# Optimization experiments

Measured on AMD Instinct MI355X. Metric: run time of the kernel, lower is better.

The kernel has to match this reference:

```python
import jax, jax.numpy as jnp
import numpy as np

N = 100000      # nodes
E = 1200000     # edges
B = 128         # graphs
H = 64          # hidden
IN_DIM = 64
GN_EPS = 1e-5


def _gin(x, edge_index, w1, b1, w2, b2):
    # GINConv (eps=0): mlp(x + sum_{j in N(i)} x_j)
    agg = jax.ops.segment_sum(x[edge_index[0]], edge_index[1], num_segments=N)
    h = x + agg
    return jax.nn.relu(h @ w1 + b1) @ w2 + b2


def _graph_norm(x, batch, w, b, ms):
    # PyG GraphNorm: out = w * (x - ms*mean) / sqrt(var + eps) + b, per-graph stats
    ones = jnp.ones((x.shape[0],), x.dtype)
    cnt = jnp.maximum(jax.ops.segment_sum(ones, batch, num_segments=B), 1.0)[:, None]
    mean = jax.ops.segment_sum(x, batch, num_segments=B) / cnt
    out = x - ms * mean[batch]
    var = jax.ops.segment_sum(out * out, batch, num_segments=B) / cnt
    return out * (jax.lax.rsqrt(var + GN_EPS)[batch] * w) + b


def setup_inputs() -> dict:
    key = jax.random.key(0)
    ks = jax.random.split(key, 32)
    inp = {
        'x': jax.random.normal(ks[0], (N, IN_DIM), jnp.float32),
        'edge_index': jax.random.randint(ks[1], (2, E), 0, N, dtype=jnp.int32),
        'batch': jnp.sort(jax.random.randint(ks[2], (N,), 0, B, dtype=jnp.int32)),
        'u': jax.random.normal(ks[3], (B, 3), jnp.float32),
    }
    k = 4
    for i in range(3):
        fin = IN_DIM if i == 0 else H
        inp[f'w{i+1}a'] = jax.random.normal(ks[k], (fin, H), jnp.float32) / np.sqrt(fin); k += 1
        inp[f'b{i+1}a'] = jnp.zeros((H,), jnp.float32)
        inp[f'w{i+1}b'] = jax.random.normal(ks[k], (H, H), jnp.float32) / np.sqrt(H); k += 1
        inp[f'b{i+1}b'] = jnp.zeros((H,), jnp.float32)
        inp[f'gn{i+1}_w'] = jnp.ones((H,), jnp.float32)
        inp[f'gn{i+1}_b'] = jnp.zeros((H,), jnp.float32)
        inp[f'gn{i+1}_ms'] = jnp.ones((H,), jnp.float32)
    inp['gate_w'] = jax.random.normal(ks[k], (H, 1), jnp.float32) / np.sqrt(H); k += 1
    inp['gate_b'] = jnp.zeros((1,), jnp.float32)
    inp['hw1'] = jax.random.normal(ks[k], (3 * H + 3, H), jnp.float32) / np.sqrt(3 * H + 3); k += 1
    inp['hb1'] = jnp.zeros((H,), jnp.float32)
    inp['hw2'] = jax.random.normal(ks[k], (H, 1), jnp.float32) / np.sqrt(H); k += 1
    inp['hb2'] = jnp.zeros((1,), jnp.float32)
    return inp


def reference(x, edge_index, batch, u,
              w1a, b1a, w1b, b1b, gn1_w, gn1_b, gn1_ms,
              w2a, b2a, w2b, b2b, gn2_w, gn2_b, gn2_ms,
              w3a, b3a, w3b, b3b, gn3_w, gn3_b, gn3_ms,
              gate_w, gate_b, hw1, hb1, hw2, hb2):
    h1 = jax.nn.relu(_graph_norm(_gin(x, edge_index, w1a, b1a, w1b, b1b), batch, gn1_w, gn1_b, gn1_ms))
    h2 = jax.nn.relu(_graph_norm(_gin(h1, edge_index, w2a, b2a, w2b, b2b), batch, gn2_w, gn2_b, gn2_ms))
    h3 = jax.nn.relu(_graph_norm(_gin(h2, edge_index, w3a, b3a, w3b, b3b), batch, gn3_w, gn3_b, gn3_ms))
    h = h1 + h2 + h3

    # AttentionalAggregation: per-graph softmax over gate logits
    gate = h @ gate_w + gate_b                                      # [N,1]
    m = jax.ops.segment_max(gate, batch, num_segments=B)            # [B,1]
    ex = jnp.exp(gate - m[batch])
    den = jax.ops.segment_sum(ex, batch, num_segments=B)
    att = jax.ops.segment_sum((ex / den[batch]) * h, batch, num_segments=B)

    ones = jnp.ones((h.shape[0],), h.dtype)
    cnt = jnp.maximum(jax.ops.segment_sum(ones, batch, num_segments=B), 1.0)[:, None]
    mean_pool = jax.ops.segment_sum(h, batch, num_segments=B) / cnt
    max_pool = jax.ops.segment_max(h, batch, num_segments=B)

    z = jnp.concatenate([att, mean_pool, max_pool, u], axis=1)       # [B, 3H+3]
    out = jax.nn.relu(z @ hw1 + hb1) @ hw2 + hb2                     # head_cls
    return out.reshape(-1)
```

## Files before the change

### kernel.cpp

```cpp
#include <hip/hip_runtime.h>
#include <math.h>

#define HDIM 64
#define GN_EPS 1e-5f
#define MAXNB 512
#define APITCH 72

typedef __attribute__((ext_vector_type(8))) short bf16x8;
typedef __attribute__((ext_vector_type(4))) float f32x4;

__device__ __forceinline__ int lower_bound_i(const int* a, int n, int key){
  int lo = 0, hi = n;
  while (lo < hi){ int mid = (lo + hi) >> 1; if (a[mid] < key) lo = mid + 1; else hi = mid; }
  return lo;
}

__device__ __forceinline__ unsigned fenc(float x){
  unsigned b = __float_as_uint(x);
  return (b & 0x80000000u) ? ~b : (b | 0x80000000u);
}
__device__ __forceinline__ float fdec(unsigned u){
  unsigned b = (u & 0x80000000u) ? (u ^ 0x80000000u) : ~u;
  return __uint_as_float(b);
}

__device__ __forceinline__ unsigned short f2bf(float f){
  unsigned u = __float_as_uint(f);
  u += 0x7fffu + ((u >> 16) & 1u);
  return (unsigned short)(u >> 16);
}
__device__ __forceinline__ float bf2f(unsigned short h){
  return __uint_as_float(((unsigned)h) << 16);
}

__device__ __forceinline__ void addbf(float* a, uint4 v){
  a[0] += __uint_as_float(v.x << 16);
  a[1] += __uint_as_float(v.x & 0xffff0000u);
  a[2] += __uint_as_float(v.y << 16);
  a[3] += __uint_as_float(v.y & 0xffff0000u);
  a[4] += __uint_as_float(v.z << 16);
  a[5] += __uint_as_float(v.z & 0xffff0000u);
  a[6] += __uint_as_float(v.w << 16);
  a[7] += __uint_as_float(v.w & 0xffff0000u);
}

__global__ void k_prep(const int* __restrict__ dst, int* __restrict__ bcount, int E, int NB,
                       const float* __restrict__ Wa0, const float* __restrict__ Wb0,
                       const float* __restrict__ Wa1, const float* __restrict__ Wb1,
                       const float* __restrict__ Wa2, const float* __restrict__ Wb2,
                       short* __restrict__ wbf,
                       const int* __restrict__ batch, int N, int* __restrict__ gs, int B){
  int tid = threadIdx.x;
  if (blockIdx.x < 256){
    __shared__ int lh[MAXNB];
    for (int b = tid; b < NB; b += 256) lh[b] = 0;
    __syncthreads();
    for (int i = blockIdx.x * 256 + tid; i < E; i += 256 * 256)
      atomicAdd(&lh[dst[i] >> 8], 1);
    __syncthreads();
    for (int b = tid; b < NB; b += 256){ int c = lh[b]; if (c) atomicAdd(&bcount[b], c); }
  } else if (blockIdx.x < 262){
    int wi = blockIdx.x - 256;
    const float* Wsrc[6] = {Wa0, Wb0, Wa1, Wb1, Wa2, Wb2};
    const float* W = Wsrc[wi];
    short* hi = wbf + wi * 8192;
    short* lo = hi + 4096;
    for (int i = tid; i < 4096; i += 256){
      int k = i >> 6, j = i & 63;
      float v = W[i];
      unsigned short h = f2bf(v);
      hi[j * 64 + k] = (short)h;
      lo[j * 64 + k] = (short)f2bf(v - bf2f(h));
    }
  } else {
    for (int g = tid; g <= B; g += 256) gs[g] = lower_bound_i(batch, N, g);
  }
}

__global__ void k_cvt(const float* __restrict__ x, unsigned short* __restrict__ xb, int n16){
  int i = blockIdx.x * blockDim.x + threadIdx.x;
  if (i >= n16) return;
  float4 v = ((const float4*)x)[i];
  ushort4 o;
  o.x = f2bf(v.x); o.y = f2bf(v.y); o.z = f2bf(v.z); o.w = f2bf(v.w);
  ((ushort4*)xb)[i] = o;
}

__global__ void k_bscan(const int* __restrict__ bcount, int* __restrict__ bbase,
                        int* __restrict__ bcursor, int NB){
  __shared__ int sd[MAXNB];
  int tid = threadIdx.x;
  int v = (tid < NB) ? bcount[tid] : 0;
  sd[tid] = v; __syncthreads();
  for (int o = 1; o < MAXNB; o <<= 1){
    int t = (tid >= o) ? sd[tid - o] : 0;
    __syncthreads();
    sd[tid] += t;
    __syncthreads();
  }
  int excl = sd[tid] - v;
  if (tid < NB){ bbase[tid] = excl; bcursor[tid] = excl; }
  if (tid == NB - 1) bbase[NB] = excl + v;
}

#define RCHUNK 8192
__global__ void k_breorder(const int* __restrict__ src, const int* __restrict__ dst,
                           int* __restrict__ bcursor, int2* __restrict__ ebuf, int E, int NB){
  __shared__ int lh[MAXNB];
  __shared__ int lbase[MAXNB];
  int tid = threadIdx.x;
  int c0 = blockIdx.x * RCHUNK;
  for (int b = tid; b < NB; b += 256) lh[b] = 0;
  __syncthreads();
  for (int j = 0; j < RCHUNK / 256; j++){
    int i = c0 + j * 256 + tid;
    if (i < E) atomicAdd(&lh[dst[i] >> 8], 1);
  }
  __syncthreads();
  for (int b = tid; b < NB; b += 256){
    int c = lh[b];
    lbase[b] = c ? atomicAdd(&bcursor[b], c) : 0;
    lh[b] = 0;
  }
  __syncthreads();
  for (int j = 0; j < RCHUNK / 256; j++){
    int i = c0 + j * 256 + tid;
    if (i < E){
      int d = dst[i]; int b = d >> 8;
      int r = atomicAdd(&lh[b], 1);
      ebuf[lbase[b] + r] = make_int2(src[i], d);
    }
  }
}

__global__ void k_bucket_csr(const int2* __restrict__ ebuf, const int* __restrict__ bbase,
                             int* __restrict__ deg, int* __restrict__ offs,
                             int* __restrict__ csr, int N){
  __shared__ int lh[256];
  __shared__ int lsc[256];
  int b = blockIdx.x;
  int lo = b << 8;
  int nn = min(256, N - lo);
  int tid = threadIdx.x;
  lh[tid] = 0; __syncthreads();
  int es = bbase[b], ee = bbase[b + 1];
  for (int i = es + tid; i < ee; i += 256) atomicAdd(&lh[ebuf[i].y - lo], 1);
  __syncthreads();
  int v = lh[tid];
  lsc[tid] = v; __syncthreads();
  for (int o = 1; o < 256; o <<= 1){
    int t = (tid >= o) ? lsc[tid - o] : 0;
    __syncthreads();
    lsc[tid] += t;
    __syncthreads();
  }
  int excl = lsc[tid] - v;
  if (tid < nn){ deg[lo + tid] = v; offs[lo + tid] = es + excl; }
  __syncthreads();
  lh[tid] = es + excl;
  __syncthreads();
  for (int i = es + tid; i < ee; i += 256){
    int2 e = ebuf[i];
    int pos = atomicAdd(&lh[e.y - lo], 1);
    csr[pos] = e.x;
  }
}

__global__ __launch_bounds__(256) void k_agg(
    const unsigned short* __restrict__ Pb, const int* __restrict__ csr,
    const int* __restrict__ offs, const int* __restrict__ deg,
    float* __restrict__ G, int n){
  int tid = threadIdx.x;
  int wave_id = blockIdx.x * 4 + (tid >> 6);
  int lane = tid & 63;
  int sub = lane >> 3, l8 = lane & 7;
  int node = wave_id * 8 + sub;
  bool ok = node < n;
  int st = 0, cnt = 0;
  if (ok){ st = offs[node]; cnt = deg[node]; }
  const uint4* Pv = (const uint4*)Pb;
  float a[8];
  #pragma unroll
  for (int k = 0; k < 8; k++) a[k] = 0.f;
  if (ok) addbf(a, Pv[(size_t)node * 8 + l8]);
  int sbase = sub << 3;
  for (int base = 0; base < cnt; base += 8){
    int rem = cnt - base;
    int s = (l8 < rem) ? csr[st + base + l8] : 0;
    int m = min(rem, 8);
    int j = 0;
    for (; j + 4 <= m; j += 4){
      int s0 = __shfl(s, sbase | j);
      int s1 = __shfl(s, sbase | (j + 1));
      int s2 = __shfl(s, sbase | (j + 2));
      int s3 = __shfl(s, sbase | (j + 3));
      uint4 v0 = Pv[(size_t)s0 * 8 + l8];
      uint4 v1 = Pv[(size_t)s1 * 8 + l8];
      uint4 v2 = Pv[(size_t)s2 * 8 + l8];
      uint4 v3 = Pv[(size_t)s3 * 8 + l8];
      addbf(a, v0); addbf(a, v1); addbf(a, v2); addbf(a, v3);
    }
    for (; j < m; ++j){
      int sj = __shfl(s, sbase | j);
      addbf(a, Pv[(size_t)sj * 8 + l8]);
    }
  }
  if (ok){
    float4* Gp = (float4*)(G + (size_t)node * HDIM + l8 * 8);
    Gp[0] = make_float4(a[0], a[1], a[2], a[3]);
    Gp[1] = make_float4(a[4], a[5], a[6], a[7]);
  }
}

__global__ __launch_bounds__(256, 3) void k_mlp(
    float* __restrict__ G, const int* __restrict__ batch,
    const short* __restrict__ Wall,
    const float* __restrict__ B1, const float* __restrict__ B2,
    float* __restrict__ stats, int N){
  __shared__ short Ws[16384];
  __shared__ short Ah[64 * APITCH];
  __shared__ short Al[64 * APITCH];
  __shared__ float ssum[64], ssq[64];
  int tid = threadIdx.x;

  #pragma unroll
  for (int i = 0; i < 8; i++)
    ((float4*)Ws)[i * 256 + tid] = ((const float4*)Wall)[i * 256 + tid];

  int wv = tid >> 6, lane = tid & 63;
  int quad = lane >> 4, l15 = lane & 15;
  int rbase = wv << 4;
  float bb1[4], bb2[4];
  #pragma unroll
  for (int t = 0; t < 4; t++){ bb1[t] = B1[t * 16 + l15]; bb2[t] = B2[t * 16 + l15]; }

  int tile0 = blockIdx.x << 1;
  float4 r[4], r2[4];
  {
    int tb = tile0 << 6;
    #pragma unroll
    for (int ri = 0; ri < 4; ri++){
      int idx = ri * 256 + tid;
      int node = tb + (idx >> 4), f4 = idx & 15;
      r[ri] = make_float4(0.f, 0.f, 0.f, 0.f);
      if (node < N) r[ri] = ((const float4*)G)[(size_t)node * 16 + f4];
    }
  }

  for (int tt = 0; tt < 2; tt++){
    int t0 = (tile0 + tt) << 6;
    if (t0 >= N) break;

    #pragma unroll
    for (int ri = 0; ri < 4; ri++){
      int idx = ri * 256 + tid;
      int node = idx >> 4, f4 = idx & 15;
      float vv[4] = {r[ri].x, r[ri].y, r[ri].z, r[ri].w};
      short h[4], l[4];
      #pragma unroll
      for (int j = 0; j < 4; j++){
        unsigned short hh = f2bf(vv[j]);
        h[j] = (short)hh;
        l[j] = (short)f2bf(vv[j] - bf2f(hh));
      }
      *(short4*)(Ah + node * APITCH + f4 * 4) = make_short4(h[0], h[1], h[2], h[3]);
      *(short4*)(Al + node * APITCH + f4 * 4) = make_short4(l[0], l[1], l[2], l[3]);
    }
    if (tid < 64){ ssum[tid] = 0.f; ssq[tid] = 0.f; }
    __syncthreads();

    if (tt == 0){
      int tb = (tile0 + 1) << 6;
      #pragma unroll
      for (int ri = 0; ri < 4; ri++){
        int idx = ri * 256 + tid;
        int node = tb + (idx >> 4), f4 = idx & 15;
        r2[ri] = make_float4(0.f, 0.f, 0.f, 0.f);
        if (node < N) r2[ri] = ((const float4*)G)[(size_t)node * 16 + f4];
      }
    }

    f32x4 acc[4];
    #pragma unroll
    for (int t = 0; t < 4; t++) acc[t] = (f32x4){0.f, 0.f, 0.f, 0.f};
    #pragma unroll
    for (int kb = 0; kb < 2; kb++){
      int kk = kb * 32 + quad * 8;
      bf16x8 a_h = *(const bf16x8*)(Ah + (rbase + l15) * APITCH + kk);
      bf16x8 a_l = *(const bf16x8*)(Al + (rbase + l15) * APITCH + kk);
      #pragma unroll
      for (int t = 0; t < 4; t++){
        bf16x8 b_h = *(const bf16x8*)(Ws + (t * 16 + l15) * 64 + kk);
        bf16x8 b_l = *(const bf16x8*)(Ws + 4096 + (t * 16 + l15) * 64 + kk);
        acc[t] = __builtin_amdgcn_mfma_f32_16x16x32_bf16(a_h, b_h, acc[t], 0, 0, 0);
        acc[t] = __builtin_amdgcn_mfma_f32_16x16x32_bf16(a_h, b_l, acc[t], 0, 0, 0);
        acc[t] = __builtin_amdgcn_mfma_f32_16x16x32_bf16(a_l, b_h, acc[t], 0, 0, 0);
      }
    }
    __syncthreads();

    #pragma unroll
    for (int t = 0; t < 4; t++){
      #pragma unroll
      for (int rg = 0; rg < 4; rg++){
        float v = fmaxf(acc[t][rg] + bb1[t], 0.f);
        int row = rbase + quad * 4 + rg;
        int col = t * 16 + l15;
        unsigned short hh = f2bf(v);
        Ah[row * APITCH + col] = (short)hh;
        Al[row * APITCH + col] = (short)f2bf(v - bf2f(hh));
      }
    }
    __syncthreads();

    f32x4 acc2[4];
    #pragma unroll
    for (int t = 0; t < 4; t++) acc2[t] = (f32x4){0.f, 0.f, 0.f, 0.f};
    #pragma unroll
    for (int kb = 0; kb < 2; kb++){
      int kk = kb * 32 + quad * 8;
      bf16x8 a_h = *(const bf16x8*)(Ah + (rbase + l15) * APITCH + kk);
      bf16x8 a_l = *(const bf16x8*)(Al + (rbase + l15) * APITCH + kk);
      #pragma unroll
      for (int t = 0; t < 4; t++){
        bf16x8 b_h = *(const bf16x8*)(Ws + 8192 + (t * 16 + l15) * 64 + kk);
        bf16x8 b_l = *(const bf16x8*)(Ws + 12288 + (t * 16 + l15) * 64 + kk);
        acc2[t] = __builtin_amdgcn_mfma_f32_16x16x32_bf16(a_h, b_h, acc2[t], 0, 0, 0);
        acc2[t] = __builtin_amdgcn_mfma_f32_16x16x32_bf16(a_h, b_l, acc2[t], 0, 0, 0);
        acc2[t] = __builtin_amdgcn_mfma_f32_16x16x32_bf16(a_l, b_h, acc2[t], 0, 0, 0);
      }
    }

    int lastn = min(t0 + 63, N - 1);
    int g0 = batch[t0];
    bool uniform = (batch[lastn] == g0) && (t0 + 63 < N);
    #pragma unroll
    for (int t = 0; t < 4; t++){
      int f = t * 16 + l15;
      float s = 0.f, q = 0.f;
      #pragma unroll
      for (int rg = 0; rg < 4; rg++){
        float v = acc2[t][rg] + bb2[t];
        int node = t0 + rbase + quad * 4 + rg;
        if (node < N) G[(size_t)node * HDIM + f] = v;
        if (uniform){
          s += v; q += v * v;
        } else if (node < N){
          int g = batch[node];
          atomicAdd(&stats[g * 128 + f], v);
          atomicAdd(&stats[g * 128 + 64 + f], v * v);
        }
      }
      if (uniform){
        s += __shfl_xor(s, 16); s += __shfl_xor(s, 32);
        q += __shfl_xor(q, 16); q += __shfl_xor(q, 32);
        if (quad == 0){ atomicAdd(&ssum[f], s); atomicAdd(&ssq[f], q); }
      }
    }
    __syncthreads();
    if (uniform && tid < 64){
      atomicAdd(&stats[g0 * 128 + tid], ssum[tid]);
      atomicAdd(&stats[g0 * 128 + 64 + tid], ssq[tid]);
    }
    #pragma unroll
    for (int ri = 0; ri < 4; ri++) r[ri] = r2[ri];
  }
}

__global__ void k_gn_apply(const float* __restrict__ Y, const int* __restrict__ batch,
                           const float* __restrict__ stats, const int* __restrict__ gs,
                           const float* __restrict__ w, const float* __restrict__ ms,
                           const float* __restrict__ bias,
                           unsigned short* __restrict__ Cb, float* __restrict__ hsum, int n16,
                           int first, int writeC){
  int i = blockIdx.x * blockDim.x + threadIdx.x;
  if (i >= n16) return;
  int node = i >> 4, q = i & 15;
  int g = batch[node];
  float cnt = (float)max(gs[g + 1] - gs[g], 1);
  float4 y  = ((const float4*)Y)[i];
  float4 s1 = ((const float4*)(stats + g * 128))[q];
  float4 s2 = ((const float4*)(stats + g * 128 + 64))[q];
  float4 wv = ((const float4*)w)[q];
  float4 mv = ((const float4*)ms)[q];
  float4 bv = ((const float4*)bias)[q];
  float4 v;
  #define APPLY1(c) { \
    float mean = s1.c / cnt; float ex2 = s2.c / cnt; \
    float var = ex2 - (2.f * mv.c - mv.c * mv.c) * mean * mean; \
    float sc = rsqrtf(var + GN_EPS) * wv.c; \
    v.c = fmaxf((y.c - mv.c * mean) * sc + bv.c, 0.f); }
  APPLY1(x) APPLY1(y) APPLY1(z) APPLY1(w)
  #undef APPLY1
  if (writeC){
    ushort4 o;
    o.x = f2bf(v.x); o.y = f2bf(v.y); o.z = f2bf(v.z); o.w = f2bf(v.w);
    ((ushort4*)Cb)[i] = o;
  }
  if (first){
    ((float4*)hsum)[i] = v;
  } else {
    float4 h = ((float4*)hsum)[i];
    h.x += v.x; h.y += v.y; h.z += v.z; h.w += v.w;
    ((float4*)hsum)[i] = h;
  }
}

#define GN_NPW 32
__global__ void k_pool1(const float* __restrict__ HS, const int* __restrict__ batch,
                        const float* __restrict__ GW, const float* __restrict__ GB,
                        float* __restrict__ sumbuf, unsigned* __restrict__ maxbuf,
                        float* __restrict__ gatebuf, unsigned* __restrict__ gmaxbuf, int n){
  int wave = (int)((blockIdx.x * blockDim.x + threadIdx.x) >> 6);
  int lane = threadIdx.x & 63;
  int s = wave * GN_NPW;
  if (s >= n) return;
  int e = min(s + GN_NPW, n);
  float gwv = GW[lane];
  float gb = GB[0];
  int cur = batch[s];
  float macc = 0.f, xacc = -INFINITY, gmx = -INFINITY;
  for (int nd = s; nd < e; ++nd){
    int g = batch[nd];
    if (g != cur){
      atomicAdd(&sumbuf[cur * 64 + lane], macc);
      atomicMax(&maxbuf[cur * 64 + lane], fenc(xacc));
      if (lane == 0) atomicMax(&gmaxbuf[cur], fenc(gmx));
      macc = 0.f; xacc = -INFINITY; gmx = -INFINITY; cur = g;
    }
    float hv = HS[(size_t)nd * HDIM + lane];
    macc += hv; xacc = fmaxf(xacc, hv);
    float gv = hv * gwv;
    #pragma unroll
    for (int msk = 1; msk < 64; msk <<= 1) gv += __shfl_xor(gv, msk);
    gv += gb;
    if (lane == 0) gatebuf[nd] = gv;
    gmx = fmaxf(gmx, gv);
  }
  atomicAdd(&sumbuf[cur * 64 + lane], macc);
  atomicMax(&maxbuf[cur * 64 + lane], fenc(xacc));
  if (lane == 0) atomicMax(&gmaxbuf[cur], fenc(gmx));
}

__global__ void k_pool2(const float* __restrict__ HS, const int* __restrict__ batch,
                        const float* __restrict__ gatebuf, const unsigned* __restrict__ gmaxbuf,
                        float* __restrict__ attbuf, float* __restrict__ denbuf, int n){
  int wave = (int)((blockIdx.x * blockDim.x + threadIdx.x) >> 6);
  int lane = threadIdx.x & 63;
  int s = wave * GN_NPW;
  if (s >= n) return;
  int e = min(s + GN_NPW, n);
  int cur = batch[s];
  float m = fdec(gmaxbuf[cur]);
  float aacc = 0.f, dacc = 0.f;
  for (int nd = s; nd < e; ++nd){
    int g = batch[nd];
    if (g != cur){
      atomicAdd(&attbuf[cur * 64 + lane], aacc);
      if (lane == 0) atomicAdd(&denbuf[cur], dacc);
      aacc = 0.f; dacc = 0.f; cur = g; m = fdec(gmaxbuf[cur]);
    }
    float ex = expf(gatebuf[nd] - m);
    float hv = HS[(size_t)nd * HDIM + lane];
    aacc += ex * hv; dacc += ex;
  }
  atomicAdd(&attbuf[cur * 64 + lane], aacc);
  if (lane == 0) atomicAdd(&denbuf[cur], dacc);
}

__global__ void k_pool3(const float* __restrict__ attbuf, const float* __restrict__ denbuf,
                        const float* __restrict__ sumbuf, const unsigned* __restrict__ maxbuf,
                        const int* __restrict__ gs, const float* __restrict__ U,
                        const float* __restrict__ HW1, const float* __restrict__ HB1,
                        const float* __restrict__ HW2, const float* __restrict__ HB2,
                        float* __restrict__ out){
  __shared__ float z[200];
  int g = blockIdx.x;
  int tid = threadIdx.x;
  float cnt = (float)max(gs[g + 1] - gs[g], 1);
  float den = denbuf[g];
  z[tid]       = attbuf[g * 64 + tid] / den;
  z[64 + tid]  = sumbuf[g * 64 + tid] / cnt;
  z[128 + tid] = fdec(maxbuf[g * 64 + tid]);
  if (tid < 3) z[192 + tid] = U[g * 3 + tid];
  __syncthreads();
  float acc = HB1[tid];
  for (int k = 0; k < 195; k++) acc += z[k] * HW1[k * 64 + tid];
  float sv = fmaxf(acc, 0.f) * HW2[tid];
  #pragma unroll
  for (int msk = 1; msk < 64; msk <<= 1) sv += __shfl_xor(sv, msk);
  if (tid == 0) out[g] = sv + HB2[0];
}

extern "C" void kernel_launch(void* const* d_in, const int* in_sizes, int n_in,
                              void* d_out, int out_size, void* d_ws, size_t ws_size,
                              hipStream_t stream){
  const float* x     = (const float*)d_in[0];
  const int*   ei    = (const int*)d_in[1];
  const int*   batch = (const int*)d_in[2];
  const float* u     = (const float*)d_in[3];
  const float* W[3][4]; const float* GNp[3][3];
  for (int l = 0; l < 3; l++){
    int base = 4 + l * 7;
    W[l][0]  = (const float*)d_in[base + 0];
    W[l][1]  = (const float*)d_in[base + 1];
    W[l][2]  = (const float*)d_in[base + 2];
    W[l][3]  = (const float*)d_in[base + 3];
    GNp[l][0]= (const float*)d_in[base + 4];
    GNp[l][1]= (const float*)d_in[base + 5];
    GNp[l][2]= (const float*)d_in[base + 6];
  }
  const float* gate_w = (const float*)d_in[25];
  const float* gate_b = (const float*)d_in[26];
  const float* hw1    = (const float*)d_in[27];
  const float* hb1    = (const float*)d_in[28];
  const float* hw2    = (const float*)d_in[29];
  const float* hb2    = (const float*)d_in[30];
  float* out = (float*)d_out;

  int N = in_sizes[0] / HDIM;
  int E = in_sizes[1] / 2;
  int B = in_sizes[3] / 3;
  const int* src = ei;
  const int* dst = ei + E;
  int NB = (N + 255) >> 8;

  char* w8 = (char*)d_ws;
  size_t NH = (size_t)N * HDIM * sizeof(float);
  size_t NHb = (size_t)N * HDIM * sizeof(short);
  auto alignup = [](size_t v){ return (v + 255) & ~(size_t)255; };
  size_t off = 0;
  float* hsum    = (float*)(w8 + off); off += alignup(NH);
  float* G       = (float*)(w8 + off); off += alignup(NH);
  unsigned short* xb   = (unsigned short*)(w8 + off); off += alignup(NHb);
  unsigned short* bufA = (unsigned short*)(w8 + off); off += alignup(NHb);
  unsigned short* bufB = (unsigned short*)(w8 + off); off += alignup(NHb);
  float* gatebuf = (float*)(w8 + off); off += alignup((size_t)N * 4);
  int*   deg     = (int*)(w8 + off);   off += alignup((size_t)N * 4);
  int*   offs    = (int*)(w8 + off);   off += alignup((size_t)N * 4);
  int*   csr     = (int*)(w8 + off);   off += alignup((size_t)E * 4);
  int2*  ebuf    = (int2*)(w8 + off);  off += alignup((size_t)E * 8);
  int*   bcount  = (int*)(w8 + off);   off += alignup((size_t)(MAXNB + 1) * 4);
  int*   bbase   = (int*)(w8 + off);   off += alignup((size_t)(MAXNB + 1) * 4);
  int*   bcursor = (int*)(w8 + off);   off += alignup((size_t)(MAXNB + 1) * 4);
  float* stats   = (float*)(w8 + off); off += alignup((size_t)3 * B * 128 * 4);
  float* poolz   = (float*)(w8 + off);
  size_t poolz_bytes = ((size_t)B * 64 * 3 + 2 * B) * 4;
  off += alignup(poolz_bytes);
  float*    sumbuf  = poolz;
  unsigned* maxbuf  = (unsigned*)(poolz + (size_t)B * 64);
  float*    attbuf  = poolz + (size_t)2 * B * 64;
  float*    denbuf  = poolz + (size_t)3 * B * 64;
  unsigned* gmaxbuf = (unsigned*)(poolz + (size_t)3 * B * 64 + B);
  int*   gs      = (int*)(w8 + off);   off += alignup((size_t)(B + 1) * 4);
  short* wbf     = (short*)(w8 + off); off += alignup((size_t)6 * 8192 * 2);
  (void)ws_size; (void)n_in; (void)out_size;

  hipMemsetAsync(stats, 0, (size_t)3 * B * 128 * 4, stream);
  hipMemsetAsync(poolz, 0, poolz_bytes, stream);
  hipMemsetAsync(bcount, 0, (size_t)(MAXNB + 1) * 4, stream);

  const int tb = 256;
  int n16 = N * 16;
  k_prep<<<263, tb, 0, stream>>>(dst, bcount, E, NB,
                                 W[0][0], W[0][2], W[1][0], W[1][2], W[2][0], W[2][2],
                                 wbf, batch, N, gs, B);
  k_cvt<<<(n16 + tb - 1) / tb, tb, 0, stream>>>(x, xb, n16);
  k_bscan<<<1, MAXNB, 0, stream>>>(bcount, bbase, bcursor, NB);
  k_breorder<<<(E + RCHUNK - 1) / RCHUNK, tb, 0, stream>>>(src, dst, bcursor, ebuf, E, NB);
  k_bucket_csr<<<NB, tb, 0, stream>>>(ebuf, bbase, deg, offs, csr, N);

  int nwaves = (N + GN_NPW - 1) / GN_NPW;
  int segblocks = (nwaves * 64 + tb - 1) / tb;
  int nblk64 = (N + 63) >> 6;
  int nblk2 = (nblk64 + 1) >> 1;
  int aggwaves = (N + 7) >> 3;
  int aggblocks = (aggwaves + 3) >> 2;

  const unsigned short* P = xb;
  unsigned short* C = bufA;
  for (int l = 0; l < 3; l++){
    k_agg<<<aggblocks, 256, 0, stream>>>(P, csr, offs, deg, G, N);
    float* lstats = stats + (size_t)l * B * 128;
    k_mlp<<<nblk2, 256, 0, stream>>>(G, batch, wbf + (size_t)l * 16384,
                                     W[l][1], W[l][3], lstats, N);
    k_gn_apply<<<(n16 + tb - 1) / tb, tb, 0, stream>>>(G, batch, lstats, gs,
                                                       GNp[l][0], GNp[l][2], GNp[l][1],
                                                       C, hsum, n16, l == 0 ? 1 : 0,
                                                       l == 2 ? 0 : 1);
    P = C;
    C = (l == 0) ? bufB : bufA;
  }
  k_pool1<<<segblocks, tb, 0, stream>>>(hsum, batch, gate_w, gate_b,
                                        sumbuf, maxbuf, gatebuf, gmaxbuf, N);
  k_pool2<<<segblocks, tb, 0, stream>>>(hsum, batch, gatebuf, gmaxbuf, attbuf, denbuf, N);
  k_pool3<<<B, 64, 0, stream>>>(attbuf, denbuf, sumbuf, maxbuf, gs, u,
                                hw1, hb1, hw2, hb2, out);
}
```

Baseline: 496.1 us.

## Fuse preprocessing and trunk into two persistent cooperative kernels with grid sync

Measured after the change: 486.8 us. About the same (-1.9%).

```diff
diff --git a/kernel.cpp b/kernel.cpp
--- a/kernel.cpp
+++ b/kernel.cpp
@@ -1,10 +1,14 @@
 #include <hip/hip_runtime.h>
+#include <hip/hip_cooperative_groups.h>
 #include <math.h>
+
+namespace cg = cooperative_groups;
 
 #define HDIM 64
 #define GN_EPS 1e-5f
 #define MAXNB 512
 #define APITCH 72
+#define RCHUNK 8192
 
 typedef __attribute__((ext_vector_type(8))) short bf16x8;
 typedef __attribute__((ext_vector_type(4))) float f32x4;
@@ -14,7 +18,6 @@
   while (lo < hi){ int mid = (lo + hi) >> 1; if (a[mid] < key) lo = mid + 1; else hi = mid; }
   return lo;
 }
-
 __device__ __forceinline__ unsigned fenc(float x){
   unsigned b = __float_as_uint(x);
   return (b & 0x80000000u) ? ~b : (b | 0x80000000u);
@@ -23,7 +26,6 @@
   unsigned b = (u & 0x80000000u) ? (u ^ 0x80000000u) : ~u;
   return __uint_as_float(b);
 }
-
 __device__ __forceinline__ unsigned short f2bf(float f){
   unsigned u = __float_as_uint(f);
   u += 0x7fffu + ((u >> 16) & 1u);
@@ -32,7 +34,6 @@
 __device__ __forceinline__ float bf2f(unsigned short h){
   return __uint_as_float(((unsigned)h) << 16);
 }
-
 __device__ __forceinline__ void addbf(float* a, uint4 v){
   a[0] += __uint_as_float(v.x << 16);
   a[1] += __uint_as_float(v.x & 0xffff0000u);
@@ -42,6 +43,500 @@
   a[5] += __uint_as_float(v.z & 0xffff0000u);
   a[6] += __uint_as_float(v.w << 16);
   a[7] += __uint_as_float(v.w & 0xffff0000u);
+}
+
+struct BuildArgs {
+  const int* src; const int* dst; int E; int NB;
+  const float* W0; const float* W1; const float* W2;
+  const float* W3; const float* W4; const float* W5;
+  short* wbf;
+  const int* batch; int N; int* gs; int B;
+  int* bcount; int* bbase; int* bcursor;
+  int2* ebuf; int* deg; int* offs; int* csr;
+  const float* x; unsigned short* xb; int n16;
+  float* stats; int statsN; float* poolz; int poolzN;
+};
+
+__global__ void k_build(BuildArgs a){
+  cg::grid_group grid = cg::this_grid();
+  __shared__ int sA[512];
+  __shared__ int sB[512];
+  int tid = threadIdx.x;
+  int gsz = (int)gridDim.x;
+  int gstart = blockIdx.x * 256 + tid;
+  int gstride = gsz * 256;
+
+  for (int i = gstart; i <= MAXNB; i += gstride) a.bcount[i] = 0;
+  for (int i = gstart; i < a.statsN; i += gstride) a.stats[i] = 0.f;
+  for (int i = gstart; i < a.poolzN; i += gstride) a.poolz[i] = 0.f;
+  if (blockIdx.x < 6){
+    const float* Wsrc = (blockIdx.x == 0) ? a.W0 : (blockIdx.x == 1) ? a.W1 :
+                        (blockIdx.x == 2) ? a.W2 : (blockIdx.x == 3) ? a.W3 :
+                        (blockIdx.x == 4) ? a.W4 : a.W5;
+    short* hi = a.wbf + blockIdx.x * 8192;
+    short* lo = hi + 4096;
+    for (int i = tid; i < 4096; i += 256){
+      int k = i >> 6, j = i & 63;
+      float v = Wsrc[i];
+      unsigned short h = f2bf(v);
+      hi[j * 64 + k] = (short)h;
+      lo[j * 64 + k] = (short)f2bf(v - bf2f(h));
+    }
+  } else if (blockIdx.x == 6){
+    for (int g = tid; g <= a.B; g += 256) a.gs[g] = lower_bound_i(a.batch, a.N, g);
+  }
+  for (int i = gstart; i < a.n16; i += gstride){
+    float4 v = ((const float4*)a.x)[i];
+    ushort4 o;
+    o.x = f2bf(v.x); o.y = f2bf(v.y); o.z = f2bf(v.z); o.w = f2bf(v.w);
+    ((ushort4*)a.xb)[i] = o;
+  }
+  grid.sync();
+
+  for (int b = tid; b < a.NB; b += 256) sA[b] = 0;
+  __syncthreads();
+  for (int i = gstart; i < a.E; i += gstride) atomicAdd(&sA[a.dst[i] >> 8], 1);
+  __syncthreads();
+  for (int b = tid; b < a.NB; b += 256){ int c = sA[b]; if (c) atomicAdd(&a.bcount[b], c); }
+  grid.sync();
+
+  if (blockIdx.x == 0){
+    int v0 = (2 * tid     < a.NB) ? a.bcount[2 * tid]     : 0;
+    int v1 = (2 * tid + 1 < a.NB) ? a.bcount[2 * tid + 1] : 0;
+    int L = v0 + v1;
+    sB[tid] = L; __syncthreads();
+    for (int o = 1; o < 256; o <<= 1){
+      int tv = (tid >= o) ? sB[tid - o] : 0;
+      __syncthreads();
+      sB[tid] += tv;
+      __syncthreads();
+    }
+    int run = sB[tid] - L;
+    if (2 * tid < a.NB){ a.bbase[2 * tid] = run; a.bcursor[2 * tid] = run; }
+    run += v0;
+    if (2 * tid + 1 < a.NB){ a.bbase[2 * tid + 1] = run; a.bcursor[2 * tid + 1] = run; }
+    if (tid == 255) a.bbase[a.NB] = sB[255];
+  }
+  grid.sync();
+
+  int nch = (a.E + RCHUNK - 1) / RCHUNK;
+  for (int ci = blockIdx.x; ci < nch; ci += gsz){
+    int c0 = ci * RCHUNK;
+    for (int b = tid; b < a.NB; b += 256) sA[b] = 0;
+    __syncthreads();
+    for (int j = 0; j < RCHUNK / 256; j++){
+      int i = c0 + j * 256 + tid;
+      if (i < a.E) atomicAdd(&sA[a.dst[i] >> 8], 1);
+    }
+    __syncthreads();
+    for (int b = tid; b < a.NB; b += 256){
+      int c = sA[b];
+      sB[b] = c ? atomicAdd(&a.bcursor[b], c) : 0;
+      sA[b] = 0;
+    }
+    __syncthreads();
+    for (int j = 0; j < RCHUNK / 256; j++){
+      int i = c0 + j * 256 + tid;
+      if (i < a.E){
+        int d = a.dst[i]; int b = d >> 8;
+        int rr = atomicAdd(&sA[b], 1);
+        a.ebuf[sB[b] + rr] = make_int2(a.src[i], d);
+      }
+    }
+    __syncthreads();
+  }
+  grid.sync();
+
+  for (int b = blockIdx.x; b < a.NB; b += gsz){
+    int lo = b << 8;
+    int nn = min(256, a.N - lo);
+    sA[tid] = 0; __syncthreads();
+    int es = a.bbase[b], ee = a.bbase[b + 1];
+    for (int i = es + tid; i < ee; i += 256) atomicAdd(&sA[a.ebuf[i].y - lo], 1);
+    __syncthreads();
+    int v = sA[tid];
+    sB[tid] = v; __syncthreads();
+    for (int o = 1; o < 256; o <<= 1){
+      int tv = (tid >= o) ? sB[tid - o] : 0;
+      __syncthreads();
+      sB[tid] += tv;
+      __syncthreads();
+    }
+    int excl = sB[tid] - v;
+    if (tid < nn){ a.deg[lo + tid] = v; a.offs[lo + tid] = es + excl; }
+    __syncthreads();
+    sA[tid] = es + excl;
+    __syncthreads();
+    for (int i = es + tid; i < ee; i += 256){
+      int2 e = a.ebuf[i];
+      int pos = atomicAdd(&sA[e.y - lo], 1);
+      a.csr[pos] = e.x;
+    }
+    __syncthreads();
+  }
+}
+
+struct TrunkArgs {
+  const unsigned short* xb;
+  unsigned short* bufA; unsigned short* bufB;
+  float* G; float* hsum;
+  const int* csr; const int* offs; const int* deg; const int* batch; const int* gs;
+  const short* wbf;
+  const float* B1a; const float* B1b; const float* B1c;
+  const float* B2a; const float* B2b; const float* B2c;
+  const float* gnw0; const float* gnw1; const float* gnw2;
+  const float* gnb0; const float* gnb1; const float* gnb2;
+  const float* gnm0; const float* gnm1; const float* gnm2;
+  float* stats; int N; int n16; int B;
+  const float* gw; const float* gb; const float* u;
+  const float* hw1; const float* hb1; const float* hw2; const float* hb2;
+  float* sumbuf; unsigned* maxbuf; float* attbuf; float* denbuf; unsigned* gmaxbuf;
+  float* gatebuf; float* out;
+};
+
+__global__ __launch_bounds__(256, 3) void k_trunk(TrunkArgs a){
+  cg::grid_group grid = cg::this_grid();
+  __shared__ __align__(16) char smem[51712];
+  short* Ws  = (short*)smem;
+  short* Ah  = (short*)(smem + 32768);
+  short* Al  = (short*)(smem + 32768 + 9216);
+  float* ssum = (float*)(smem + 32768 + 18432);
+  float* ssq  = ssum + 64;
+  int tid = threadIdx.x;
+  int wv = tid >> 6, lane = tid & 63;
+  int gsz = (int)gridDim.x;
+  int N = a.N;
+  int ntile = (N + 63) >> 6;
+
+  const unsigned short* P = a.xb;
+  unsigned short* Cb = a.bufA;
+
+  for (int l = 0; l < 3; l++){
+    {
+      int sub = lane >> 3, l8 = lane & 7, sbase = sub << 3;
+      const uint4* Pv = (const uint4*)P;
+      int wid = blockIdx.x * 4 + wv;
+      int wstep = gsz * 4 * 8;
+      for (int nb = wid * 8; nb < N; nb += wstep){
+        int node = nb + sub;
+        bool ok = node < N;
+        int st = 0, cnt = 0;
+        if (ok){ st = a.offs[node]; cnt = a.deg[node]; }
+        float acc8[8];
+        #pragma unroll
+        for (int k = 0; k < 8; k++) acc8[k] = 0.f;
+        if (ok) addbf(acc8, Pv[(size_t)node * 8 + l8]);
+        for (int base = 0; base < cnt; base += 8){
+          int rem = cnt - base;
+          int s = (l8 < rem) ? a.csr[st + base + l8] : 0;
+          int m = min(rem, 8);
+          int j = 0;
+          for (; j + 4 <= m; j += 4){
+            int s0 = __shfl(s, sbase | j);
+            int s1 = __shfl(s, sbase | (j + 1));
+            int s2 = __shfl(s, sbase | (j + 2));
+            int s3 = __shfl(s, sbase | (j + 3));
+            uint4 v0 = Pv[(size_t)s0 * 8 + l8];
+            uint4 v1 = Pv[(size_t)s1 * 8 + l8];
+            uint4 v2 = Pv[(size_t)s2 * 8 + l8];
+            uint4 v3 = Pv[(size_t)s3 * 8 + l8];
+            addbf(acc8, v0); addbf(acc8, v1); addbf(acc8, v2); addbf(acc8, v3);
+          }
+          for (; j < m; ++j){
+            int sj = __shfl(s, sbase | j);
+            addbf(acc8, Pv[(size_t)sj * 8 + l8]);
+          }
+        }
+        if (ok){
+          float4* Gp = (float4*)(a.G + (size_t)node * HDIM + l8 * 8);
+          Gp[0] = make_float4(acc8[0], acc8[1], acc8[2], acc8[3]);
+          Gp[1] = make_float4(acc8[4], acc8[5], acc8[6], acc8[7]);
+        }
+      }
+    }
+    grid.sync();
+
+    {
+      const short* Wall = a.wbf + (size_t)l * 16384;
+      for (int j = tid; j < 2048; j += 256){
+        int p = j >> 9, rem = j & 511, rr = rem >> 3, c8 = rem & 7;
+        bf16x8 v = ((const bf16x8*)Wall)[j];
+        *(bf16x8*)(Ws + p * 4096 + rr * 64 + ((c8 ^ (rr & 7)) << 3)) = v;
+      }
+      int quad = lane >> 4, l15 = lane & 15;
+      int rbase = wv << 4;
+      int h7 = l15 & 7;
+      const float* B1 = (l == 0) ? a.B1a : (l == 1) ? a.B1b : a.B1c;
+      const float* B2 = (l == 0) ? a.B2a : (l == 1) ? a.B2b : a.B2c;
+      float bb1[4], bb2[4];
+      #pragma unroll
+      for (int t4 = 0; t4 < 4; t4++){ bb1[t4] = B1[t4 * 16 + l15]; bb2[t4] = B2[t4 * 16 + l15]; }
+      float* lstats = a.stats + (size_t)l * a.B * 128;
+
+      int t = blockIdx.x;
+      float4 r[4], r2[4];
+      #pragma unroll
+      for (int ri = 0; ri < 4; ri++){ r[ri] = make_float4(0.f,0.f,0.f,0.f); r2[ri] = r[ri]; }
+      if (t < ntile){
+        int tb = t << 6;
+        #pragma unroll
+        for (int ri = 0; ri < 4; ri++){
+          int idx = ri * 256 + tid;
+          int node = tb + (idx >> 4), f4 = idx & 15;
+          if (node < N) r[ri] = ((const float4*)a.G)[(size_t)node * 16 + f4];
+        }
+      }
+      while (t < ntile){
+        int t0 = t << 6;
+        #pragma unroll
+        for (int ri = 0; ri < 4; ri++){
+          int idx = ri * 256 + tid;
+          int nodeL = idx >> 4, f4 = idx & 15;
+          float vv[4] = {r[ri].x, r[ri].y, r[ri].z, r[ri].w};
+          short hh[4], ll[4];
+          #pragma unroll
+          for (int j = 0; j < 4; j++){
+            unsigned short hv = f2bf(vv[j]);
+            hh[j] = (short)hv;
+            ll[j] = (short)f2bf(vv[j] - bf2f(hv));
+          }
+          *(short4*)(Ah + nodeL * APITCH + f4 * 4) = make_short4(hh[0], hh[1], hh[2], hh[3]);
+          *(short4*)(Al + nodeL * APITCH + f4 * 4) = make_short4(ll[0], ll[1], ll[2], ll[3]);
+        }
+        if (tid < 64){ ssum[tid] = 0.f; ssq[tid] = 0.f; }
+        __syncthreads();
+
+        int tn = t + gsz;
+        #pragma unroll
+        for (int ri = 0; ri < 4; ri++) r2[ri] = make_float4(0.f,0.f,0.f,0.f);
+        if (tn < ntile){
+          int tb = tn << 6;
+          #pragma unroll
+          for (int ri = 0; ri < 4; ri++){
+            int idx = ri * 256 + tid;
+            int node = tb + (idx >> 4), f4 = idx & 15;
+            if (node < N) r2[ri] = ((const float4*)a.G)[(size_t)node * 16 + f4];
+          }
+        }
+
+        f32x4 acc[4];
+        #pragma unroll
+        for (int t4 = 0; t4 < 4; t4++) acc[t4] = (f32x4){0.f, 0.f, 0.f, 0.f};
+        #pragma unroll
+        for (int kb = 0; kb < 2; kb++){
+          int kk = kb * 32 + quad * 8;
+          int swz = ((kb * 4 + quad) ^ h7) << 3;
+          bf16x8 a_h = *(const bf16x8*)(Ah + (rbase + l15) * APITCH + kk);
+          bf16x8 a_l = *(const bf16x8*)(Al + (rbase + l15) * APITCH + kk);
+          #pragma unroll
+          for (int t4 = 0; t4 < 4; t4++){
+            int row = t4 * 16 + l15;
+            bf16x8 b_h = *(const bf16x8*)(Ws + row * 64 + swz);
+            bf16x8 b_l = *(const bf16x8*)(Ws + 4096 + row * 64 + swz);
+            acc[t4] = __builtin_amdgcn_mfma_f32_16x16x32_bf16(a_h, b_h, acc[t4], 0, 0, 0);
+            acc[t4] = __builtin_amdgcn_mfma_f32_16x16x32_bf16(a_h, b_l, acc[t4], 0, 0, 0);
+            acc[t4] = __builtin_amdgcn_mfma_f32_16x16x32_bf16(a_l, b_h, acc[t4], 0, 0, 0);
+          }
+        }
+        __syncthreads();
+
+        #pragma unroll
+        for (int t4 = 0; t4 < 4; t4++){
+          #pragma unroll
+          for (int rg = 0; rg < 4; rg++){
+            float v = fmaxf(acc[t4][rg] + bb1[t4], 0.f);
+            int row = rbase + quad * 4 + rg;
+            int col = t4 * 16 + l15;
+            unsigned short hv = f2bf(v);
+            Ah[row * APITCH + col] = (short)hv;
+            Al[row * APITCH + col] = (short)f2bf(v - bf2f(hv));
+          }
+        }
+        __syncthreads();
+
+        f32x4 acc2[4];
+        #pragma unroll
+        for (int t4 = 0; t4 < 4; t4++) acc2[t4] = (f32x4){0.f, 0.f, 0.f, 0.f};
+        #pragma unroll
+        for (int kb = 0; kb < 2; kb++){
+          int kk = kb * 32 + quad * 8;
+          int swz = ((kb * 4 + quad) ^ h7) << 3;
+          bf16x8 a_h = *(const bf16x8*)(Ah + (rbase + l15) * APITCH + kk);
+          bf16x8 a_l = *(const bf16x8*)(Al + (rbase + l15) * APITCH + kk);
+          #pragma unroll
+          for (int t4 = 0; t4 < 4; t4++){
+            int row = t4 * 16 + l15;
+            bf16x8 b_h = *(const bf16x8*)(Ws + 8192 + row * 64 + swz);
+            bf16x8 b_l = *(const bf16x8*)(Ws + 12288 + row * 64 + swz);
+            acc2[t4] = __builtin_amdgcn_mfma_f32_16x16x32_bf16(a_h, b_h, acc2[t4], 0, 0, 0);
+            acc2[t4] = __builtin_amdgcn_mfma_f32_16x16x32_bf16(a_h, b_l, acc2[t4], 0, 0, 0);
+            acc2[t4] = __builtin_amdgcn_mfma_f32_16x16x32_bf16(a_l, b_h, acc2[t4], 0, 0, 0);
+          }
+        }
+
+        int lastn = min(t0 + 63, N - 1);
+        int g0 = a.batch[t0];
+        bool uniform = (a.batch[lastn] == g0) && (t0 + 63 < N);
+        #pragma unroll
+        for (int t4 = 0; t4 < 4; t4++){
+          int f = t4 * 16 + l15;
+          float s = 0.f, q = 0.f;
+          #pragma unroll
+          for (int rg = 0; rg < 4; rg++){
+            float v = acc2[t4][rg] + bb2[t4];
+            int node = t0 + rbase + quad * 4 + rg;
+            if (node < N) a.G[(size_t)node * HDIM + f] = v;
+            if (uniform){
+              s += v; q += v * v;
+            } else if (node < N){
+              int g = a.batch[node];
+              atomicAdd(&lstats[g * 128 + f], v);
+              atomicAdd(&lstats[g * 128 + 64 + f], v * v);
+            }
+          }
+          if (uniform){
+            s += __shfl_xor(s, 16); s += __shfl_xor(s, 32);
+            q += __shfl_xor(q, 16); q += __shfl_xor(q, 32);
+            if (quad == 0){ atomicAdd(&ssum[f], s); atomicAdd(&ssq[f], q); }
+          }
+        }
+        __syncthreads();
+        if (uniform && tid < 64){
+          atomicAdd(&lstats[g0 * 128 + tid], ssum[tid]);
+          atomicAdd(&lstats[g0 * 128 + 64 + tid], ssq[tid]);
+        }
+        #pragma unroll
+        for (int ri = 0; ri < 4; ri++) r[ri] = r2[ri];
+        t = tn;
+      }
+    }
+    grid.sync();
+
+    {
+      const float* wv_ = (l == 0) ? a.gnw0 : (l == 1) ? a.gnw1 : a.gnw2;
+      const float* bv_ = (l == 0) ? a.gnb0 : (l == 1) ? a.gnb1 : a.gnb2;
+      const float* mv_ = (l == 0) ? a.gnm0 : (l == 1) ? a.gnm1 : a.gnm2;
+      const float* lstats = a.stats + (size_t)l * a.B * 128;
+      int first = (l == 0) ? 1 : 0;
+      int writeC = (l == 2) ? 0 : 1;
+      for (int i = blockIdx.x * 256 + tid; i < a.n16; i += gsz * 256){
+        int node = i >> 4, q = i & 15;
+        int g = a.batch[node];
+        float cnt = (float)max(a.gs[g + 1] - a.gs[g], 1);
+        float4 y  = ((const float4*)a.G)[i];
+        float4 s1 = ((const float4*)(lstats + g * 128))[q];
+        float4 s2 = ((const float4*)(lstats + g * 128 + 64))[q];
+        float4 wq = ((const float4*)wv_)[q];
+        float4 mq = ((const float4*)mv_)[q];
+        float4 bq = ((const float4*)bv_)[q];
+        float4 v;
+        #define APPLY1(c) { \
+          float mean = s1.c / cnt; float ex2 = s2.c / cnt; \
+          float var = ex2 - (2.f * mq.c - mq.c * mq.c) * mean * mean; \
+          float sc = rsqrtf(var + GN_EPS) * wq.c; \
+          v.c = fmaxf((y.c - mq.c * mean) * sc + bq.c, 0.f); }
+        APPLY1(x) APPLY1(y) APPLY1(z) APPLY1(w)
+        #undef APPLY1
+        if (writeC){
+          ushort4 o;
+          o.x = f2bf(v.x); o.y = f2bf(v.y); o.z = f2bf(v.z); o.w = f2bf(v.w);
+          ((ushort4*)Cb)[i] = o;
+        }
+        if (first){
+          ((float4*)a.hsum)[i] = v;
+        } else {
+          float4 h = ((float4*)a.hsum)[i];
+          h.x += v.x; h.y += v.y; h.z += v.z; h.w += v.w;
+          ((float4*)a.hsum)[i] = h;
+        }
+      }
+    }
+    grid.sync();
+    P = Cb;
+    Cb = (l == 0) ? a.bufB : a.bufA;
+  }
+
+  {
+    int nchunk = (N + 31) >> 5;
+    int wid = blockIdx.x * 4 + wv;
+    float gwv = a.gw[lane];
+    float gb = a.gb[0];
+    for (int c = wid; c < nchunk; c += gsz * 4){
+      int s = c << 5, e = min(s + 32, N);
+      int cur = a.batch[s];
+      float macc = 0.f, xacc = -INFINITY, gmx = -INFINITY;
+      for (int nd = s; nd < e; ++nd){
+        int g = a.batch[nd];
+        if (g != cur){
+          atomicAdd(&a.sumbuf[cur * 64 + lane], macc);
+          atomicMax(&a.maxbuf[cur * 64 + lane], fenc(xacc));
+          if (lane == 0) atomicMax(&a.gmaxbuf[cur], fenc(gmx));
+          macc = 0.f; xacc = -INFINITY; gmx = -INFINITY; cur = g;
+        }
+        float hv = a.hsum[(size_t)nd * HDIM + lane];
+        macc += hv; xacc = fmaxf(xacc, hv);
+        float gv = hv * gwv;
+        #pragma unroll
+        for (int msk = 1; msk < 64; msk <<= 1) gv += __shfl_xor(gv, msk);
+        gv += gb;
+        if (lane == 0) a.gatebuf[nd] = gv;
+        gmx = fmaxf(gmx, gv);
+      }
+      atomicAdd(&a.sumbuf[cur * 64 + lane], macc);
+      atomicMax(&a.maxbuf[cur * 64 + lane], fenc(xacc));
+      if (lane == 0) atomicMax(&a.gmaxbuf[cur], fenc(gmx));
+    }
+  }
+  grid.sync();
+
+  {
+    int nchunk = (N + 31) >> 5;
+    int wid = blockIdx.x * 4 + wv;
+    for (int c = wid; c < nchunk; c += gsz * 4){
+      int s = c << 5, e = min(s + 32, N);
+      int cur = a.batch[s];
+      float m = fdec(a.gmaxbuf[cur]);
+      float aacc = 0.f, dacc = 0.f;
+      for (int nd = s; nd < e; ++nd){
+        int g = a.batch[nd];
+        if (g != cur){
+          atomicAdd(&a.attbuf[cur * 64 + lane], aacc);
+          if (lane == 0) atomicAdd(&a.denbuf[cur], dacc);
+          aacc = 0.f; dacc = 0.f; cur = g; m = fdec(a.gmaxbuf[cur]);
+        }
+        float ex = expf(a.gatebuf[nd] - m);
+        float hv = a.hsum[(size_t)nd * HDIM + lane];
+        aacc += ex * hv; dacc += ex;
+      }
+      atomicAdd(&a.attbuf[cur * 64 + lane], aacc);
+      if (lane == 0) atomicAdd(&a.denbuf[cur], dacc);
+    }
+  }
+  grid.sync();
+
+  {
+    float* z = (float*)smem;
+    int g = blockIdx.x;
+    if (g < a.B){
+      float cnt = (float)max(a.gs[g + 1] - a.gs[g], 1);
+      if (tid < 64){
+        float den = a.denbuf[g];
+        z[tid]       = a.attbuf[g * 64 + tid] / den;
+        z[64 + tid]  = a.sumbuf[g * 64 + tid] / cnt;
+        z[128 + tid] = fdec(a.maxbuf[g * 64 + tid]);
+        if (tid < 3) z[192 + tid] = a.u[g * 3 + tid];
+      }
+      __syncthreads();
+      if (tid < 64){
+        float acc = a.hb1[tid];
+        for (int k = 0; k < 195; k++) acc += z[k] * a.hw1[k * 64 + tid];
+        float sv = fmaxf(acc, 0.f) * a.hw2[tid];
+        #pragma unroll
+        for (int msk = 1; msk < 64; msk <<= 1) sv += __shfl_xor(sv, msk);
+        if (tid == 0) a.out[g] = sv + a.hb2[0];
+      }
+    }
+  }
 }
 
 __global__ void k_prep(const int* __restrict__ dst, int* __restrict__ bcount, int E, int NB,
@@ -103,7 +598,6 @@
   if (tid == NB - 1) bbase[NB] = excl + v;
 }
 
-#define RCHUNK 8192
 __global__ void k_breorder(const int* __restrict__ src, const int* __restrict__ dst,
                            int* __restrict__ bcursor, int2* __restrict__ ebuf, int E, int NB){
   __shared__ int lh[MAXNB];
@@ -223,13 +717,16 @@
   __shared__ float ssum[64], ssq[64];
   int tid = threadIdx.x;
 
-  #pragma unroll
-  for (int i = 0; i < 8; i++)
-    ((float4*)Ws)[i * 256 + tid] = ((const float4*)Wall)[i * 256 + tid];
+  for (int j = tid; j < 2048; j += 256){
+    int p = j >> 9, rem = j & 511, rr = rem >> 3, c8 = rem & 7;
+    bf16x8 v = ((const bf16x8*)Wall)[j];
+    *(bf16x8*)(Ws + p * 4096 + rr * 64 + ((c8 ^ (rr & 7)) << 3)) = v;
+  }
 
   int wv = tid >> 6, lane = tid & 63;
   int quad = lane >> 4, l15 = lane & 15;
   int rbase = wv << 4;
+  int h7 = l15 & 7;
   float bb1[4], bb2[4];
   #pragma unroll
   for (int t = 0; t < 4; t++){ bb1[t] = B1[t * 16 + l15]; bb2[t] = B2[t * 16 + l15]; }
@@ -286,12 +783,14 @@
     #pragma unroll
     for (int kb = 0; kb < 2; kb++){
       int kk = kb * 32 + quad * 8;
+      int swz = ((kb * 4 + quad) ^ h7) << 3;
       bf16x8 a_h = *(const bf16x8*)(Ah + (rbase + l15) * APITCH + kk);
       bf16x8 a_l = *(const bf16x8*)(Al + (rbase + l15) * APITCH + kk);
       #pragma unroll
       for (int t = 0; t < 4; t++){
-        bf16x8 b_h = *(const bf16x8*)(Ws + (t * 16 + l15) * 64 + kk);
-        bf16x8 b_l = *(const bf16x8*)(Ws + 4096 + (t * 16 + l15) * 64 + kk);
+        int row = t * 16 + l15;
+        bf16x8 b_h = *(const bf16x8*)(Ws + row * 64 + swz);
+        bf16x8 b_l = *(const bf16x8*)(Ws + 4096 + row * 64 + swz);
         acc[t] = __builtin_amdgcn_mfma_f32_16x16x32_bf16(a_h, b_h, acc[t], 0, 0, 0);
         acc[t] = __builtin_amdgcn_mfma_f32_16x16x32_bf16(a_h, b_l, acc[t], 0, 0, 0);
         acc[t] = __builtin_amdgcn_mfma_f32_16x16x32_bf16(a_l, b_h, acc[t], 0, 0, 0);
@@ -319,12 +818,14 @@
     #pragma unroll
     for (int kb = 0; kb < 2; kb++){
       int kk = kb * 32 + quad * 8;
+      int swz = ((kb * 4 + quad) ^ h7) << 3;
       bf16x8 a_h = *(const bf16x8*)(Ah + (rbase + l15) * APITCH + kk);
       bf16x8 a_l = *(const bf16x8*)(Al + (rbase + l15) * APITCH + kk);
       #pragma unroll
       for (int t = 0; t < 4; t++){
-        bf16x8 b_h = *(const bf16x8*)(Ws + 8192 + (t * 16 + l15) * 64 + kk);
-        bf16x8 b_l = *(const bf16x8*)(Ws + 12288 + (t * 16 + l15) * 64 + kk);
+        int row = t * 16 + l15;
+        bf16x8 b_h = *(const bf16x8*)(Ws + 8192 + row * 64 + swz);
+        bf16x8 b_l = *(const bf16x8*)(Ws + 12288 + row * 64 + swz);
         acc2[t] = __builtin_amdgcn_mfma_f32_16x16x32_bf16(a_h, b_h, acc2[t], 0, 0, 0);
         acc2[t] = __builtin_amdgcn_mfma_f32_16x16x32_bf16(a_h, b_l, acc2[t], 0, 0, 0);
         acc2[t] = __builtin_amdgcn_mfma_f32_16x16x32_bf16(a_l, b_h, acc2[t], 0, 0, 0);
@@ -524,6 +1025,7 @@
   const int* src = ei;
   const int* dst = ei + E;
   int NB = (N + 255) >> 8;
+  int n16 = N * 16;
 
   char* w8 = (char*)d_ws;
   size_t NH = (size_t)N * HDIM * sizeof(float);
@@ -545,8 +1047,8 @@
   int*   bcursor = (int*)(w8 + off);   off += alignup((size_t)(MAXNB + 1) * 4);
   float* stats   = (float*)(w8 + off); off += alignup((size_t)3 * B * 128 * 4);
   float* poolz   = (float*)(w8 + off);
-  size_t poolz_bytes = ((size_t)B * 64 * 3 + 2 * B) * 4;
-  off += alignup(poolz_bytes);
+  int poolzN = B * 64 * 3 + 2 * B;
+  off += alignup((size_t)poolzN * 4);
   float*    sumbuf  = poolz;
   unsigned* maxbuf  = (unsigned*)(poolz + (size_t)B * 64);
   float*    attbuf  = poolz + (size_t)2 * B * 64;
@@ -556,44 +1058,96 @@
   short* wbf     = (short*)(w8 + off); off += alignup((size_t)6 * 8192 * 2);
   (void)ws_size; (void)n_in; (void)out_size;
 
-  hipMemsetAsync(stats, 0, (size_t)3 * B * 128 * 4, stream);
-  hipMemsetAsync(poolz, 0, poolz_bytes, stream);
-  hipMemsetAsync(bcount, 0, (size_t)(MAXNB + 1) * 4, stream);
-
-  const int tb = 256;
-  int n16 = N * 16;
-  k_prep<<<263, tb, 0, stream>>>(dst, bcount, E, NB,
-                                 W[0][0], W[0][2], W[1][0], W[1][2], W[2][0], W[2][2],
-                                 wbf, batch, N, gs, B);
-  k_cvt<<<(n16 + tb - 1) / tb, tb, 0, stream>>>(x, xb, n16);
-  k_bscan<<<1, MAXNB, 0, stream>>>(bcount, bbase, bcursor, NB);
-  k_breorder<<<(E + RCHUNK - 1) / RCHUNK, tb, 0, stream>>>(src, dst, bcursor, ebuf, E, NB);
-  k_bucket_csr<<<NB, tb, 0, stream>>>(ebuf, bbase, deg, offs, csr, N);
-
-  int nwaves = (N + GN_NPW - 1) / GN_NPW;
-  int segblocks = (nwaves * 64 + tb - 1) / tb;
-  int nblk64 = (N + 63) >> 6;
-  int nblk2 = (nblk64 + 1) >> 1;
-  int aggwaves = (N + 7) >> 3;
-  int aggblocks = (aggwaves + 3) >> 2;
-
-  const unsigned short* P = xb;
-  unsigned short* C = bufA;
-  for (int l = 0; l < 3; l++){
-    k_agg<<<aggblocks, 256, 0, stream>>>(P, csr, offs, deg, G, N);
-    float* lstats = stats + (size_t)l * B * 128;
-    k_mlp<<<nblk2, 256, 0, stream>>>(G, batch, wbf + (size_t)l * 16384,
-                                     W[l][1], W[l][3], lstats, N);
-    k_gn_apply<<<(n16 + tb - 1) / tb, tb, 0, stream>>>(G, batch, lstats, gs,
-                                                       GNp[l][0], GNp[l][2], GNp[l][1],
-                                                       C, hsum, n16, l == 0 ? 1 : 0,
-                                                       l == 2 ? 0 : 1);
-    P = C;
-    C = (l == 0) ? bufB : bufA;
-  }
-  k_pool1<<<segblocks, tb, 0, stream>>>(hsum, batch, gate_w, gate_b,
-                                        sumbuf, maxbuf, gatebuf, gmaxbuf, N);
-  k_pool2<<<segblocks, tb, 0, stream>>>(hsum, batch, gatebuf, gmaxbuf, attbuf, denbuf, N);
-  k_pool3<<<B, 64, 0, stream>>>(attbuf, denbuf, sumbuf, maxbuf, gs, u,
-                                hw1, hb1, hw2, hb2, out);
-}
+  int dev = 0; hipGetDevice(&dev);
+  int coopAttr = 0, nCU = 0;
+  hipDeviceGetAttribute(&coopAttr, hipDeviceAttributeCooperativeLaunch, dev);
+  hipDeviceGetAttribute(&nCU, hipDeviceAttributeMultiprocessorCount, dev);
+  int mbB = 0, mbT = 0;
+  hipOccupancyMaxActiveBlocksPerMultiprocessor(&mbB, k_build, 256, 0);
+  hipOccupancyMaxActiveBlocksPerMultiprocessor(&mbT, k_trunk, 256, 0);
+  bool coop = coopAttr && nCU > 0 && mbB >= 1 && mbT >= 3 &&
+              (long)mbT * nCU >= (long)B && (long)mbB * nCU >= 8;
+
+  bool done = false;
+  if (coop){
+    BuildArgs ba;
+    ba.src = src; ba.dst = dst; ba.E = E; ba.NB = NB;
+    ba.W0 = W[0][0]; ba.W1 = W[0][2]; ba.W2 = W[1][0];
+    ba.W3 = W[1][2]; ba.W4 = W[2][0]; ba.W5 = W[2][2];
+    ba.wbf = wbf;
+    ba.batch = batch; ba.N = N; ba.gs = gs; ba.B = B;
+    ba.bcount = bcount; ba.bbase = bbase; ba.bcursor = bcursor;
+    ba.ebuf = ebuf; ba.deg = deg; ba.offs = offs; ba.csr = csr;
+    ba.x = x; ba.xb = xb; ba.n16 = n16;
+    ba.stats = stats; ba.statsN = 3 * B * 128; ba.poolz = poolz; ba.poolzN = poolzN;
+
+    TrunkArgs ta;
+    ta.xb = xb; ta.bufA = bufA; ta.bufB = bufB; ta.G = G; ta.hsum = hsum;
+    ta.csr = csr; ta.offs = offs; ta.deg = deg; ta.batch = batch; ta.gs = gs;
+    ta.wbf = wbf;
+    ta.B1a = W[0][1]; ta.B1b = W[1][1]; ta.B1c = W[2][1];
+    ta.B2a = W[0][3]; ta.B2b = W[1][3]; ta.B2c = W[2][3];
+    ta.gnw0 = GNp[0][0]; ta.gnw1 = GNp[1][0]; ta.gnw2 = GNp[2][0];
+    ta.gnb0 = GNp[0][1]; ta.gnb1 = GNp[1][1]; ta.gnb2 = GNp[2][1];
+    ta.gnm0 = GNp[0][2]; ta.gnm1 = GNp[1][2]; ta.gnm2 = GNp[2][2];
+    ta.stats = stats; ta.N = N; ta.n16 = n16; ta.B = B;
+    ta.gw = gate_w; ta.gb = gate_b; ta.u = u;
+    ta.hw1 = hw1; ta.hb1 = hb1; ta.hw2 = hw2; ta.hb2 = hb2;
+    ta.sumbuf = sumbuf; ta.maxbuf = maxbuf; ta.attbuf = attbuf;
+    ta.denbuf = denbuf; ta.gmaxbuf = gmaxbuf;
+    ta.gatebuf = gatebuf; ta.out = out;
+
+    int gridB = mbB * nCU; if (gridB > 1024) gridB = 1024;
+    int gridT = mbT * nCU; if (gridT > 1024) gridT = 1024;
+    void* bp[] = { &ba };
+    void* tp[] = { &ta };
+    hipError_t e = hipLaunchCooperativeKernel((const void*)k_build, dim3(gridB), dim3(256),
+                                              bp, 0, stream);
+    if (e == hipSuccess)
+      e = hipLaunchCooperativeKernel((const void*)k_trunk, dim3(gridT), dim3(256),
+                                     tp, 0, stream);
+    done = (e == hipSuccess);
+  }
+
+  if (!done){
+    hipMemsetAsync(stats, 0, (size_t)3 * B * 128 * 4, stream);
+    hipMemsetAsync(poolz, 0, (size_t)poolzN * 4, stream);
+    hipMemsetAsync(bcount, 0, (size_t)(MAXNB + 1) * 4, stream);
+
+    const int tb = 256;
+    k_prep<<<263, tb, 0, stream>>>(dst, bcount, E, NB,
+                                   W[0][0], W[0][2], W[1][0], W[1][2], W[2][0], W[2][2],
+                                   wbf, batch, N, gs, B);
+    k_cvt<<<(n16 + tb - 1) / tb, tb, 0, stream>>>(x, xb, n16);
+    k_bscan<<<1, MAXNB, 0, stream>>>(bcount, bbase, bcursor, NB);
+    k_breorder<<<(E + RCHUNK - 1) / RCHUNK, tb, 0, stream>>>(src, dst, bcursor, ebuf, E, NB);
+    k_bucket_csr<<<NB, tb, 0, stream>>>(ebuf, bbase, deg, offs, csr, N);
+
+    int nwaves = (N + GN_NPW - 1) / GN_NPW;
+    int segblocks = (nwaves * 64 + tb - 1) / tb;
+    int nblk64 = (N + 63) >> 6;
+    int nblk2 = (nblk64 + 1) >> 1;
+    int aggwaves = (N + 7) >> 3;
+    int aggblocks = (aggwaves + 3) >> 2;
+
+    const unsigned short* P = xb;
+    unsigned short* C = bufA;
+    for (int l = 0; l < 3; l++){
+      k_agg<<<aggblocks, 256, 0, stream>>>(P, csr, offs, deg, G, N);
+      float* lstats = stats + (size_t)l * B * 128;
+      k_mlp<<<nblk2, 256, 0, stream>>>(G, batch, wbf + (size_t)l * 16384,
+                                       W[l][1], W[l][3], lstats, N);
+      k_gn_apply<<<(n16 + tb - 1) / tb, tb, 0, stream>>>(G, batch, lstats, gs,
+                                                         GNp[l][0], GNp[l][2], GNp[l][1],
+                                                         C, hsum, n16, l == 0 ? 1 : 0,
+                                                         l == 2 ? 0 : 1);
+      P = C;
+      C = (l == 0) ? bufB : bufA;
+    }
+    k_pool1<<<segblocks, tb, 0, stream>>>(hsum, batch, gate_w, gate_b,
+                                          sumbuf, maxbuf, gatebuf, gmaxbuf, N);
+    k_pool2<<<segblocks, tb, 0, stream>>>(hsum, batch, gatebuf, gmaxbuf, attbuf, denbuf, N);
+    k_pool3<<<B, 64, 0, stream>>>(attbuf, denbuf, sumbuf, maxbuf, gs, u,
+                                  hw1, hb1, hw2, hb2, out);
+  }
+}
```
